# Optimization experiments

Measured on AMD Instinct MI355X. Metric: run time of the kernel, lower is better.

## Reference

```python
import jax, jax.numpy as jnp
import numpy as np

B, D = 4096, 1024
N_CLASSES = 100
INF = jnp.float32(3.4e38)


def setup_inputs() -> dict:
    key = jax.random.key(0)
    k1, k2 = jax.random.split(key)
    x = jax.random.normal(k1, (B, 1, D), dtype=jnp.float32)
    labels = jax.random.randint(k2, (B,), 0, N_CLASSES)
    return {"x": x, "labels": labels}


def _awareness_scan(xs, labels_f, R_init):
    # xs: [B, D] float32, labels_f: [B] float32
    b, d = xs.shape
    slots = jnp.arange(b)

    def step(state, inp):
        refs, ref_labels, n_refs, count, min_d, max_d, R = state
        xi, li = inp
        mask = slots < n_refs  # active reference slots
        # distances from candidate to current reference set (torch.cdist, p=2)
        d_all = jnp.sqrt(jnp.sum((refs - xi[None, :]) ** 2, axis=-1))  # [B]
        d_all = jax.lax.stop_gradient(d_all)
        d_act = jnp.where(mask, d_all, INF)
        min_act = jnp.min(d_act)
        is_first = count == 1
        # new reference iff ALL active distances exceed R (i.e. min > R)
        insert = is_first | (min_act > R)
        refs2 = jnp.where(insert, refs.at[n_refs].set(xi), refs)
        ref_labels2 = jnp.where(insert, ref_labels.at[n_refs].set(li), ref_labels)
        n_refs2 = n_refs + insert.astype(n_refs.dtype)
        # dynamic ray update (skipped on the very first sample, as in torch)
        max_act = jnp.max(jnp.where(mask, d_all, -INF))
        min_d2 = jnp.where(is_first, min_d, jnp.minimum(min_d, min_act))
        max_d2 = jnp.where(is_first, max_d, jnp.maximum(max_d, max_act))
        R2 = jnp.where(is_first, R, (min_d2 + max_d2) / 3)
        # prediction: nearest reference AFTER potential insertion
        mask2 = slots < n_refs2
        d2 = jnp.sqrt(jnp.sum((refs2 - xi[None, :]) ** 2, axis=-1))
        d2 = jax.lax.stop_gradient(d2)
        idx = jnp.argmin(jnp.where(mask2, d2, INF))
        pred = ref_labels2[idx]
        new_state = (refs2, ref_labels2, n_refs2, count + 1, min_d2, max_d2, R2)
        return new_state, pred

    init = (
        jnp.zeros((b, d), jnp.float32),   # reference instances buffer
        jnp.zeros((b,), jnp.float32),     # reference labels buffer
        jnp.int32(0),                     # n_refs
        jnp.int32(1),                     # count (starts at 1, as in torch)
        INF,                              # min_dist
        jnp.float32(0.0),                 # max_dist
        jnp.float32(R_init),              # R
    )
    _, preds = jax.lax.scan(step, init, (xs, labels_f))
    return preds  # [B] float32


def reference(x, labels):
    # x: [B, 1, D]; labels: [B] int. update_ref_insts=True, set_labels=labels.
    xs = x.reshape(x.shape[0], x.shape[2])
    labels_f = labels.astype(jnp.float32)
    return _awareness_scan(xs, labels_f, 1.0)
```

## Files before the change

kernel.cpp:

```cpp
#include <hip/hip_runtime.h>
#include <stdint.h>

#define B_N   4096
#define D_DIM 1024
#define INF_F 3.4e38f

typedef float floatx4 __attribute__((ext_vector_type(4)));

#define XQ_OFF 131072

__global__ __launch_bounds__(256)
void k_prep(const float* __restrict__ x, unsigned char* __restrict__ xq,
            float* __restrict__ norms,
            unsigned long long* __restrict__ minpack,
            unsigned int* __restrict__ maxbits) {
    const int row = blockIdx.x;
    const int t   = threadIdx.x;
    float4 v = ((const float4*)x)[row * 256 + t];
    int p = __builtin_amdgcn_cvt_pk_fp8_f32(v.x, v.y, 0, false);
    p     = __builtin_amdgcn_cvt_pk_fp8_f32(v.z, v.w, p, true);
    ((int*)xq)[row * 256 + t] = p;
    float s = v.x * v.x + v.y * v.y + v.z * v.z + v.w * v.w;
    #pragma unroll
    for (int off = 32; off; off >>= 1) s += __shfl_down(s, off);
    __shared__ float ws4[4];
    if ((t & 63) == 0) ws4[t >> 6] = s;
    __syncthreads();
    if (t == 0) {
        norms[row]   = ws4[0] + ws4[1] + ws4[2] + ws4[3];
        minpack[row] = 0xFFFFFFFFFFFFFFFFull;
        maxbits[row] = 0u;
    }
}

#define GLDS(g, l)                                                              \
    __builtin_amdgcn_global_load_lds(                                           \
        (__attribute__((address_space(1))) void*)(void*)(g),                    \
        (__attribute__((address_space(3))) void*)(void*)(l), 16, 0, 0)

__global__ __launch_bounds__(256, 3)
void k_pass1_fp8(const unsigned char* __restrict__ xq,
                 const float* __restrict__ norms,
                 unsigned long long* __restrict__ minpack,
                 unsigned int* __restrict__ maxbits) {
    int bid = blockIdx.x;
    int ti  = (int)((sqrtf(8.f * bid + 1.f) - 1.f) * 0.5f);
    while ((ti + 1) * (ti + 2) / 2 <= bid) ti++;
    while (ti * (ti + 1) / 2 > bid) ti--;
    int tj  = bid - ti * (ti + 1) / 2;

    __shared__ unsigned char As[16384];
    __shared__ unsigned char Bs[16384];
    __shared__ unsigned long long redMin[128][2];
    __shared__ float redMax[128][2];

    const int t    = threadIdx.x;
    const int w    = t >> 6, lane = t & 63;
    const int wm   = w >> 1, wn = w & 1;
    const int q4   = lane >> 4, c15 = lane & 15;
    const int i0   = ti * 128, j0 = tj * 128;

    const int sr = lane >> 3;
    const int sc = (lane & 7) ^ (sr & 7);

    const unsigned char* gA[4]; const unsigned char* gB[4];
    unsigned char* lA[4]; unsigned char* lB[4];
    #pragma unroll
    for (int q = 0; q < 4; q++) {
        int e   = w * 4 + q;
        int row = e * 8 + sr;
        gA[q] = xq + (size_t)(i0 + row) * D_DIM + sc * 16;
        gB[q] = xq + (size_t)(j0 + row) * D_DIM + sc * 16;
        lA[q] = As + e * 1024;
        lB[q] = Bs + e * 1024;
    }

    const int r7 = c15 & 7;
    int oib[4];
    #pragma unroll
    for (int kk = 0; kk < 4; kk++) {
        int sl  = kk * 2 + (q4 >> 1);
        oib[kk] = (((sl ^ r7) << 4) | ((q4 & 1) << 3));
    }
    int rbA[4], rbB[4];
    #pragma unroll
    for (int st = 0; st < 4; st++) {
        rbA[st] = (wm * 64 + st * 16 + c15) * 128;
        rbB[st] = (wn * 64 + st * 16 + c15) * 128;
    }

    floatx4 acc[4][4];
    #pragma unroll
    for (int m = 0; m < 4; m++)
        #pragma unroll
        for (int n = 0; n < 4; n++)
            acc[m][n] = (floatx4){0.f, 0.f, 0.f, 0.f};

    for (int it = 0; it < 8; it++) {
        __syncthreads();
        #pragma unroll
        for (int q = 0; q < 4; q++) {
            GLDS(gA[q], lA[q]);
            GLDS(gB[q], lB[q]);
            gA[q] += 128; gB[q] += 128;
        }
        __syncthreads();
        #pragma unroll
        for (int kk = 0; kk < 4; kk++) {
            long long af[4], bfr[4];
            #pragma unroll
            for (int st = 0; st < 4; st++) {
                af[st]  = *(const long long*)(As + rbA[st] + oib[kk]);
                bfr[st] = *(const long long*)(Bs + rbB[st] + oib[kk]);
            }
            #pragma unroll
            for (int m = 0; m < 4; m++)
                #pragma unroll
                for (int n = 0; n < 4; n++)
                    acc[m][n] = __builtin_amdgcn_mfma_f32_16x16x32_fp8_fp8(
                        af[m], bfr[n], acc[m][n], 0, 0, 0);
        }
    }

    float nj[4];
    #pragma unroll
    for (int st = 0; st < 4; st++) nj[st] = norms[j0 + wn * 64 + st * 16 + c15];

    #pragma unroll
    for (int st_m = 0; st_m < 4; st_m++) {
        #pragma unroll
        for (int r = 0; r < 4; r++) {
            int i_loc = wm * 64 + st_m * 16 + q4 * 4 + r;
            int gi    = i0 + i_loc;
            float ni  = norms[gi];
            unsigned long long mp = 0xFFFFFFFFFFFFFFFFull;
            float mx = -INF_F;
            #pragma unroll
            for (int st_n = 0; st_n < 4; st_n++) {
                int gj = j0 + wn * 64 + st_n * 16 + c15;
                if (gj < gi) {
                    float dot = acc[st_m][st_n][r];
                    float d   = sqrtf(fmaxf(ni + nj[st_n] - 2.f * dot, 0.f));
                    unsigned long long p =
                        ((unsigned long long)__float_as_uint(d) << 32) | (unsigned)gj;
                    if (p < mp) mp = p;
                    mx = fmaxf(mx, d);
                }
            }
            #pragma unroll
            for (int off = 1; off < 16; off <<= 1) {
                unsigned long long op = __shfl_xor(mp, off, 64);
                if (op < mp) mp = op;
                float om = __shfl_xor(mx, off, 64);
                mx = fmaxf(mx, om);
            }
            if (c15 == 0) { redMin[i_loc][wn] = mp; redMax[i_loc][wn] = mx; }
        }
    }
    __syncthreads();
    if (t < 128) {
        unsigned long long mp = redMin[t][0];
        if (redMin[t][1] < mp) mp = redMin[t][1];
        float mx = fmaxf(redMax[t][0], redMax[t][1]);
        if (mp != 0xFFFFFFFFFFFFFFFFull) {
            atomicMin(&minpack[i0 + t], mp);
            atomicMax(&maxbits[i0 + t], __float_as_uint(mx));
        }
    }
}

__global__ __launch_bounds__(1024)
void k_tail(const unsigned long long* __restrict__ minpack,
            const unsigned int* __restrict__ maxbits,
            const float* __restrict__ x, const float* __restrict__ norms,
            const int* __restrict__ labels, int* __restrict__ ref_idx,
            float* __restrict__ out) {
    const int t = threadIdx.x;
    float m[4], M[4];
    #pragma unroll
    for (int q = 0; q < 4; q++) {
        int i = t * 4 + q;
        unsigned long long p = minpack[i];
        float dmin = (p == 0xFFFFFFFFFFFFFFFFull)
                       ? INF_F : __uint_as_float((unsigned)(p >> 32));
        m[q] = (i == 0) ? INF_F : dmin;
        M[q] = (i == 0) ? -INF_F : __uint_as_float(maxbits[i]);
    }
    float pmin[4], pmax[4];
    pmin[0] = m[0]; pmax[0] = M[0];
    #pragma unroll
    for (int q = 1; q < 4; q++) {
        pmin[q] = fminf(pmin[q - 1], m[q]);
        pmax[q] = fmaxf(pmax[q - 1], M[q]);
    }
    __shared__ float smin[1024], smax[1024];
    smin[t] = pmin[3]; smax[t] = pmax[3];
    __syncthreads();
    for (int off = 1; off < 1024; off <<= 1) {
        float a = (t >= off) ? smin[t - off] : INF_F;
        float b = (t >= off) ? smax[t - off] : -INF_F;
        __syncthreads();
        smin[t] = fminf(smin[t], a);
        smax[t] = fmaxf(smax[t], b);
        __syncthreads();
    }
    float exMin = (t > 0) ? smin[t - 1] : INF_F;
    float exMax = (t > 0) ? smax[t - 1] : -INF_F;

    int viol = B_N;
    #pragma unroll
    for (int q = 0; q < 4; q++) {
        int i = t * 4 + q;
        if (i >= 1) {
            float pm = (q == 0) ? exMin : fminf(exMin, pmin[q - 1]);
            float pM = (q == 0) ? exMax : fmaxf(exMax, pmax[q - 1]);
            float R  = (i == 1) ? 1.0f : (pm + pM) / 3.0f;
            if (!(m[q] > R) && i < viol) viol = i;
        }
    }
    __shared__ int sv[1024];
    sv[t] = viol;
    __syncthreads();
    for (int off = 512; off; off >>= 1) {
        if (t < off) sv[t] = min(sv[t], sv[t + off]);
        __syncthreads();
    }
    const int s_star = sv[0];

    for (int i = t; i < s_star; i += 1024) out[i] = (float)labels[i];

    __shared__ float s_state[3];
    __shared__ int s_n;
    if (s_star < B_N && t == (s_star >> 2)) {
        int q = s_star & 3;
        float pm = (q == 0) ? exMin : fminf(exMin, pmin[q - 1]);
        float pM = (q == 0) ? exMax : fmaxf(exMax, pmax[q - 1]);
        float md = fminf(pm, m[q]);
        float Md = fmaxf(pM, M[q]);
        s_state[0] = md; s_state[1] = Md; s_state[2] = (md + Md) / 3.0f;
        s_n = s_star;
        unsigned long long p = minpack[s_star];
        int j = (int)(unsigned)(p & 0xFFFFFFFFu);
        out[s_star] = (float)labels[j];
    }
    if (s_star >= B_N) return;

    for (int s = t; s < s_star; s += 1024) ref_idx[s] = s;
    __syncthreads();

    __shared__ unsigned long long redp[1024];
    __shared__ float redm[1024];
    for (int i = s_star + 1; i < B_N; i++) {
        int n = s_n;
        const float* xi = x + (size_t)i * D_DIM;
        float ni = norms[i];
        unsigned long long mp = 0xFFFFFFFFFFFFFFFFull;
        float mx = -INF_F;
        for (int slot = t; slot < n; slot += 1024) {
            int j = ref_idx[slot];
            const float* xj = x + (size_t)j * D_DIM;
            float dot = 0.f;
            for (int k = 0; k < D_DIM; k++) dot = fmaf(xi[k], xj[k], dot);
            float d = sqrtf(fmaxf(ni + norms[j] - 2.f * dot, 0.f));
            unsigned long long p =
                ((unsigned long long)__float_as_uint(d) << 32) | (unsigned)slot;
            if (p < mp) mp = p;
            mx = fmaxf(mx, d);
        }
        redp[t] = mp; redm[t] = mx;
        __syncthreads();
        for (int off = 512; off; off >>= 1) {
            if (t < off) {
                if (redp[t + off] < redp[t]) redp[t] = redp[t + off];
                redm[t] = fmaxf(redm[t], redm[t + off]);
            }
            __syncthreads();
        }
        if (t == 0) {
            unsigned long long p = redp[0];
            float min_act = __uint_as_float((unsigned)(p >> 32));
            int minslot   = (int)(unsigned)(p & 0xFFFFFFFFu);
            float max_act = redm[0];
            bool insert = (min_act > s_state[2]);
            int pred;
            if (insert) {
                ref_idx[n] = i;
                s_n = n + 1;
                pred = (min_act <= 0.0f) ? labels[ref_idx[minslot]] : labels[i];
            } else {
                pred = labels[ref_idx[minslot]];
            }
            float md = fminf(s_state[0], min_act);
            float Md = fmaxf(s_state[1], max_act);
            s_state[0] = md; s_state[1] = Md; s_state[2] = (md + Md) / 3.0f;
            out[i] = (float)pred;
        }
        __syncthreads();
    }
}

extern "C" void kernel_launch(void* const* d_in, const int* in_sizes, int n_in,
                              void* d_out, int out_size, void* d_ws, size_t ws_size,
                              hipStream_t stream) {
    const float* x      = (const float*)d_in[0];
    const int*   labels = (const int*)d_in[1];
    float*       out    = (float*)d_out;
    char* ws = (char*)d_ws;
    unsigned long long* minpack = (unsigned long long*)ws;
    unsigned int*       maxbits = (unsigned int*)(ws + 32768);
    float*              norms   = (float*)(ws + 49152);
    int*                ref_idx = (int*)(ws + 65600);
    unsigned char*      xq      = (unsigned char*)(ws + XQ_OFF);

    k_prep<<<B_N, 256, 0, stream>>>(x, xq, norms, minpack, maxbits);
    const int ntiles  = B_N / 128;
    const int nblocks = ntiles * (ntiles + 1) / 2;
    k_pass1_fp8<<<nblocks, 256, 0, stream>>>(xq, norms, minpack, maxbits);
    k_tail<<<1, 1024, 0, stream>>>(minpack, maxbits, x, norms, labels, ref_idx, out);
}
```

Before: 100.4 us.

## Double-buffer LDS tiles in pass1, defer sqrt to tail, use wave-shuffle scans

The FP8 pairwise-distance kernel now double-buffers its A/B LDS tiles. It prefetches the next K slice with global_load_lds while MFMAs consume the current one, synchronising through explicit vmcnt waits and barriers, and occupancy drops from 3 to 2 blocks. Squared distances are packed and reduced, and the sqrt moves to the tail kernel, which removes per-element sqrt from the epilogue. The tail kernel's prefix min/max scan and min reduction now use wave shuffles plus a small shared array instead of log-step shared-memory loops with many barriers. The cost is more LDS per block and lower occupancy.

```diff
diff --git a/kernel.cpp b/kernel.cpp
--- a/kernel.cpp
+++ b/kernel.cpp
@@ -38,7 +38,7 @@
         (__attribute__((address_space(1))) void*)(void*)(g),                    \
         (__attribute__((address_space(3))) void*)(void*)(l), 16, 0, 0)
 
-__global__ __launch_bounds__(256, 3)
+__global__ __launch_bounds__(256, 2)
 void k_pass1_fp8(const unsigned char* __restrict__ xq,
                  const float* __restrict__ norms,
                  unsigned long long* __restrict__ minpack,
@@ -49,8 +49,8 @@
     while (ti * (ti + 1) / 2 > bid) ti--;
     int tj  = bid - ti * (ti + 1) / 2;
 
-    __shared__ unsigned char As[16384];
-    __shared__ unsigned char Bs[16384];
+    __shared__ unsigned char As[2][16384];
+    __shared__ unsigned char Bs[2][16384];
     __shared__ unsigned long long redMin[128][2];
     __shared__ float redMax[128][2];
 
@@ -64,15 +64,14 @@
     const int sc = (lane & 7) ^ (sr & 7);
 
     const unsigned char* gA[4]; const unsigned char* gB[4];
-    unsigned char* lA[4]; unsigned char* lB[4];
+    int eoff[4];
     #pragma unroll
     for (int q = 0; q < 4; q++) {
         int e   = w * 4 + q;
         int row = e * 8 + sr;
         gA[q] = xq + (size_t)(i0 + row) * D_DIM + sc * 16;
         gB[q] = xq + (size_t)(j0 + row) * D_DIM + sc * 16;
-        lA[q] = As + e * 1024;
-        lB[q] = Bs + e * 1024;
+        eoff[q] = e * 1024;
     }
 
     const int r7 = c15 & 7;
@@ -96,22 +95,38 @@
         for (int n = 0; n < 4; n++)
             acc[m][n] = (floatx4){0.f, 0.f, 0.f, 0.f};
 
+    #pragma unroll
+    for (int q = 0; q < 4; q++) {
+        GLDS(gA[q], As[0] + eoff[q]);
+        GLDS(gB[q], Bs[0] + eoff[q]);
+        gA[q] += 128; gB[q] += 128;
+    }
+
+    #pragma unroll 2
     for (int it = 0; it < 8; it++) {
-        __syncthreads();
-        #pragma unroll
-        for (int q = 0; q < 4; q++) {
-            GLDS(gA[q], lA[q]);
-            GLDS(gB[q], lB[q]);
-            gA[q] += 128; gB[q] += 128;
-        }
-        __syncthreads();
+        const int p = it & 1;
+        if (it < 7) {
+            #pragma unroll
+            for (int q = 0; q < 4; q++) {
+                GLDS(gA[q], As[p ^ 1] + eoff[q]);
+                GLDS(gB[q], Bs[p ^ 1] + eoff[q]);
+                gA[q] += 128; gB[q] += 128;
+            }
+            asm volatile("s_waitcnt vmcnt(8)" ::: "memory");
+        } else {
+            asm volatile("s_waitcnt vmcnt(0)" ::: "memory");
+        }
+        __builtin_amdgcn_s_barrier();
+
+        const unsigned char* Ap = As[p];
+        const unsigned char* Bp = Bs[p];
         #pragma unroll
         for (int kk = 0; kk < 4; kk++) {
             long long af[4], bfr[4];
             #pragma unroll
             for (int st = 0; st < 4; st++) {
-                af[st]  = *(const long long*)(As + rbA[st] + oib[kk]);
-                bfr[st] = *(const long long*)(Bs + rbB[st] + oib[kk]);
+                af[st]  = *(const long long*)(Ap + rbA[st] + oib[kk]);
+                bfr[st] = *(const long long*)(Bp + rbB[st] + oib[kk]);
             }
             #pragma unroll
             for (int m = 0; m < 4; m++)
@@ -120,6 +135,8 @@
                     acc[m][n] = __builtin_amdgcn_mfma_f32_16x16x32_fp8_fp8(
                         af[m], bfr[n], acc[m][n], 0, 0, 0);
         }
+        asm volatile("s_waitcnt lgkmcnt(0)" ::: "memory");
+        __builtin_amdgcn_s_barrier();
     }
 
     float nj[4];
@@ -140,11 +157,11 @@
                 int gj = j0 + wn * 64 + st_n * 16 + c15;
                 if (gj < gi) {
                     float dot = acc[st_m][st_n][r];
-                    float d   = sqrtf(fmaxf(ni + nj[st_n] - 2.f * dot, 0.f));
+                    float d2  = fmaxf(ni + nj[st_n] - 2.f * dot, 0.f);
                     unsigned long long p =
-                        ((unsigned long long)__float_as_uint(d) << 32) | (unsigned)gj;
+                        ((unsigned long long)__float_as_uint(d2) << 32) | (unsigned)gj;
                     if (p < mp) mp = p;
-                    mx = fmaxf(mx, d);
+                    mx = fmaxf(mx, d2);
                 }
             }
             #pragma unroll
@@ -175,16 +192,17 @@
             const float* __restrict__ x, const float* __restrict__ norms,
             const int* __restrict__ labels, int* __restrict__ ref_idx,
             float* __restrict__ out) {
-    const int t = threadIdx.x;
+    const int t    = threadIdx.x;
+    const int lane = t & 63, wid = t >> 6;
     float m[4], M[4];
     #pragma unroll
     for (int q = 0; q < 4; q++) {
         int i = t * 4 + q;
         unsigned long long p = minpack[i];
         float dmin = (p == 0xFFFFFFFFFFFFFFFFull)
-                       ? INF_F : __uint_as_float((unsigned)(p >> 32));
+                       ? INF_F : sqrtf(__uint_as_float((unsigned)(p >> 32)));
         m[q] = (i == 0) ? INF_F : dmin;
-        M[q] = (i == 0) ? -INF_F : __uint_as_float(maxbits[i]);
+        M[q] = (i == 0) ? -INF_F : sqrtf(__uint_as_float(maxbits[i]));
     }
     float pmin[4], pmax[4];
     pmin[0] = m[0]; pmax[0] = M[0];
@@ -193,19 +211,25 @@
         pmin[q] = fminf(pmin[q - 1], m[q]);
         pmax[q] = fmaxf(pmax[q - 1], M[q]);
     }
-    __shared__ float smin[1024], smax[1024];
-    smin[t] = pmin[3]; smax[t] = pmax[3];
-    __syncthreads();
-    for (int off = 1; off < 1024; off <<= 1) {
-        float a = (t >= off) ? smin[t - off] : INF_F;
-        float b = (t >= off) ? smax[t - off] : -INF_F;
-        __syncthreads();
-        smin[t] = fminf(smin[t], a);
-        smax[t] = fmaxf(smax[t], b);
-        __syncthreads();
-    }
-    float exMin = (t > 0) ? smin[t - 1] : INF_F;
-    float exMax = (t > 0) ? smax[t - 1] : -INF_F;
+    float wmin = pmin[3], wmax = pmax[3];
+    #pragma unroll
+    for (int off = 1; off < 64; off <<= 1) {
+        float a = __shfl_up(wmin, off, 64);
+        float b = __shfl_up(wmax, off, 64);
+        if (lane >= off) { wmin = fminf(wmin, a); wmax = fmaxf(wmax, b); }
+    }
+    __shared__ float swmin[16], swmax[16];
+    if (lane == 63) { swmin[wid] = wmin; swmax[wid] = wmax; }
+    __syncthreads();
+    float exwMin = INF_F, exwMax = -INF_F;
+    for (int k = 0; k < wid; k++) {
+        exwMin = fminf(exwMin, swmin[k]);
+        exwMax = fmaxf(exwMax, swmax[k]);
+    }
+    float upMin = __shfl_up(wmin, 1, 64);
+    float upMax = __shfl_up(wmax, 1, 64);
+    float exMin = fminf(exwMin, (lane > 0) ? upMin : INF_F);
+    float exMax = fmaxf(exwMax, (lane > 0) ? upMax : -INF_F);
 
     int viol = B_N;
     #pragma unroll
@@ -218,14 +242,14 @@
             if (!(m[q] > R) && i < viol) viol = i;
         }
     }
-    __shared__ int sv[1024];
-    sv[t] = viol;
-    __syncthreads();
-    for (int off = 512; off; off >>= 1) {
-        if (t < off) sv[t] = min(sv[t], sv[t + off]);
-        __syncthreads();
-    }
-    const int s_star = sv[0];
+    int vw = viol;
+    #pragma unroll
+    for (int off = 32; off; off >>= 1) vw = min(vw, __shfl_down(vw, off, 64));
+    __shared__ int svw[16];
+    if (lane == 0) svw[wid] = vw;
+    __syncthreads();
+    int s_star = B_N;
+    for (int k = 0; k < 16; k++) s_star = min(s_star, svw[k]);
 
     for (int i = t; i < s_star; i += 1024) out[i] = (float)labels[i];
 
```

Result: slower. 105.8 us (+5.4%).
